# Optimization experiments

Hardware: AMD Instinct MI355X
Metric: run time of the kernel (lower is better)

The kernel has to match this reference:

```python
import jax, jax.numpy as jnp
import numpy as np

DECAY = 0.99
EPS = 1e-05


def setup_inputs() -> dict:
    key = jax.random.key(0)
    k1, k2 = jax.random.split(key)
    B, C, H, W = 16, 64, 32, 32
    K = 8192
    z_e = jax.random.normal(k1, (B, C, H, W), dtype=jnp.float32)
    embedding = jax.random.normal(k2, (K, C), dtype=jnp.float32)
    cluster_size = jnp.zeros((K,), dtype=jnp.float32)
    embedding_avg = embedding  # initialized as a clone of the codebook
    return {"z_e": z_e, "embedding": embedding, "cluster_size": cluster_size,
            "embedding_avg": embedding_avg}


def reference(z_e, embedding, cluster_size, embedding_avg):
    B, C, H, W = z_e.shape
    K = embedding.shape[0]
    # [N, C] tokens
    z_flat = jnp.transpose(z_e, (0, 2, 3, 1)).reshape(-1, C)
    d = ((z_flat * z_flat).sum(-1, keepdims=True)
         - 2.0 * (z_flat @ embedding.T)
         + (embedding * embedding).sum(-1))
    indices = jnp.argmin(d, axis=1)  # [N] int
    z_q_flat = embedding[indices]    # [N, C]
    z_q = jnp.transpose(z_q_flat.reshape(B, H, W, C), (0, 3, 1, 2))
    # EMA codebook update (training path); one-hot matmuls expressed as segment sums
    counts = jax.ops.segment_sum(jnp.ones(z_flat.shape[0], dtype=z_flat.dtype),
                                 indices, num_segments=K)            # encodings.sum(0)
    dw = jax.ops.segment_sum(z_flat, indices, num_segments=K)        # encodings.T @ z_flat
    new_cluster_size = DECAY * cluster_size + (1.0 - DECAY) * counts
    new_embedding_avg = DECAY * embedding_avg + (1.0 - DECAY) * dw
    n = new_cluster_size.sum()
    cs = (new_cluster_size + EPS) / (n + K * EPS) * n
    new_embedding = new_embedding_avg / cs[:, None]
    # straight-through estimator
    z_q_st = z_e + jax.lax.stop_gradient(z_q - z_e)
    return (z_q_st, indices.reshape(B, H * W), z_q,
            new_embedding, new_cluster_size, new_embedding_avg)
```

## Files before the change

### kernel.cpp

```cpp
#include <hip/hip_runtime.h>

#define DECAYF 0.99f
#define OMDF   0.01f
#define TAU    6.0e-3f

typedef unsigned int u32;
typedef unsigned long long u64;
typedef __attribute__((ext_vector_type(8))) short bf16x8;
typedef __attribute__((ext_vector_type(16))) float f32x16;

#define EN_OFF     0
#define EFRAG_OFF  32768
#define IDX_OFF    32768
#define LIST_OFF   98304
#define CELL_OFF   163840
#define BEST1_OFF  2129920
#define BEST2_OFF  4227072
#define CNT_OFF    5275648

__device__ __forceinline__ u64 enc_pair(float s, int idx) {
  u32 u = __float_as_uint(s);
  u = (u & 0x80000000u) ? ~u : (u | 0x80000000u);
  return ((u64)u << 32) | (u32)(~idx);
}
__device__ __forceinline__ float dec_score(u64 e) {
  u32 u = (u32)(e >> 32);
  u = (u & 0x80000000u) ? (u & 0x7fffffffu) : ~u;
  return __uint_as_float(u);
}
__device__ __forceinline__ int dec_idx(u64 e) { return (int)(~(u32)e); }
__device__ __forceinline__ unsigned short f2bf(float f) {
  u32 u = __float_as_uint(f);
  u += 0x7fffu + ((u >> 16) & 1u);
  return (unsigned short)(u >> 16);
}
__device__ __forceinline__ float exact_dot(const float* __restrict__ sx,
                                           const float* __restrict__ emb, int k) {
  const float4* e = (const float4*)(emb + (size_t)k * 64);
  float a = 0.f;
#pragma unroll
  for (int q = 0; q < 16; ++q) {
    float4 v = e[q];
    a = fmaf(sx[4 * q],     v.x, a);
    a = fmaf(sx[4 * q + 1], v.y, a);
    a = fmaf(sx[4 * q + 2], v.z, a);
    a = fmaf(sx[4 * q + 3], v.w, a);
  }
  return a;
}

__global__ __launch_bounds__(256) void k_en_eprep(const float* __restrict__ emb,
                                                  float* __restrict__ en,
                                                  unsigned char* __restrict__ efrag,
                                                  int* __restrict__ cnt,
                                                  float* __restrict__ nsum) {
  int tid = blockIdx.x * 256 + threadIdx.x;
  if (tid == 0) { *cnt = 0; *nsum = 0.f; }
  int k = tid >> 4, q = tid & 15;
  float4 v = ((const float4*)emb)[tid];
  int kstep = q >> 2, h = (q >> 1) & 1, j0 = (q & 1) * 4;
  int tile = k >> 5, n32 = k & 31;
  ushort4 hi, lo;
  hi.x = f2bf(v.x); lo.x = f2bf(v.x - __uint_as_float((u32)hi.x << 16));
  hi.y = f2bf(v.y); lo.y = f2bf(v.y - __uint_as_float((u32)hi.y << 16));
  hi.z = f2bf(v.z); lo.z = f2bf(v.z - __uint_as_float((u32)hi.z << 16));
  hi.w = f2bf(v.w); lo.w = f2bf(v.w - __uint_as_float((u32)hi.w << 16));
  size_t off = (size_t)tile * 8192 + (size_t)(kstep * 2) * 1024
             + (size_t)h * 512 + (size_t)n32 * 16 + (size_t)j0 * 2;
  *(ushort4*)(efrag + off)        = hi;
  *(ushort4*)(efrag + off + 1024) = lo;
  float s = v.x * v.x + v.y * v.y + v.z * v.z + v.w * v.w;
  s += __shfl_xor(s, 1, 16);
  s += __shfl_xor(s, 2, 16);
  s += __shfl_xor(s, 4, 16);
  s += __shfl_xor(s, 8, 16);
  if (q == 0) en[k] = 0.5f * s;
}

__global__ __launch_bounds__(256) void k_init(const float* __restrict__ cs_in,
                                              const float* __restrict__ avg_in,
                                              float* __restrict__ out4,
                                              float* __restrict__ out5,
                                              float* __restrict__ nsum) {
  int tid = blockIdx.x * 256 + threadIdx.x;
  if (tid < 131072) {
    float4 v = ((const float4*)avg_in)[tid];
    v.x *= DECAYF; v.y *= DECAYF; v.z *= DECAYF; v.w *= DECAYF;
    ((float4*)out5)[tid] = v;
  } else {
    int t = tid - 131072;
    float4 v = ((const float4*)cs_in)[t];
    v.x *= DECAYF; v.y *= DECAYF; v.z *= DECAYF; v.w *= DECAYF;
    ((float4*)out4)[t] = v;
    float s = v.x + v.y + v.z + v.w;
    s += __shfl_xor(s, 1, 64);
    s += __shfl_xor(s, 2, 64);
    s += __shfl_xor(s, 4, 64);
    s += __shfl_xor(s, 8, 64);
    s += __shfl_xor(s, 16, 64);
    s += __shfl_xor(s, 32, 64);
    if ((threadIdx.x & 63) == 0) atomicAdd(nsum, s);
  }
}

__global__ __launch_bounds__(256) void k_argmin_mfma(
    const float* __restrict__ z_e, const unsigned char* __restrict__ efrag,
    const float* __restrict__ en, u64* __restrict__ best1,
    float* __restrict__ best2) {
  alignas(16) __shared__ unsigned char sbuf[16384];
  const int tb = blockIdx.x >> 4;
  const int sl = blockIdx.x & 15;
  const int wave = threadIdx.x >> 6, lane = threadIdx.x & 63;
  const int h = lane >> 5, m = lane & 31;
  const int token0 = tb * 128 + wave * 32;

  bf16x8 ahi[4], alo[4];
  {
    const int token = token0 + m;
    const float* zp = z_e + ((size_t)(token >> 10) << 16) + (token & 1023);
#pragma unroll
    for (int ks = 0; ks < 4; ++ks) {
#pragma unroll
      for (int j = 0; j < 8; ++j) {
        int c = ks * 16 + h * 8 + j;
        float x = zp[(size_t)c << 10];
        unsigned short xh = f2bf(x);
        ahi[ks][j] = (short)xh;
        alo[ks][j] = (short)f2bf(x - __uint_as_float((u32)xh << 16));
      }
    }
  }
  float b1[16], b2[16];
#pragma unroll
  for (int r = 0; r < 16; ++r) { b1[r] = -3.0e38f; b2[r] = -3.0e38f; }

  const int scb = sl * 512;
  const unsigned char* gbase0 = efrag + (size_t)scb * 256;
  for (int ib = 0; ib < 8; ++ib) {
    const unsigned char* g = gbase0 + (size_t)ib * 16384 + (size_t)wave * 4096;
#pragma unroll
    for (int it = 0; it < 4; ++it) {
      __builtin_amdgcn_global_load_lds(
          (const __attribute__((address_space(1))) u32*)(g + it * 1024 + lane * 16),
          (__attribute__((address_space(3))) u32*)(sbuf + wave * 4096 + it * 1024),
          16, 0, 0);
    }
    __syncthreads();
#pragma unroll
    for (int t32 = 0; t32 < 2; ++t32) {
      const int t = ib * 2 + t32;
      const float negen = -en[scb + t * 32 + m];
      f32x16 acc;
#pragma unroll
      for (int r = 0; r < 16; ++r) acc[r] = negen;
      const unsigned char* sb = sbuf + t32 * 8192 + h * 512 + m * 16;
#pragma unroll
      for (int ks = 0; ks < 4; ++ks) {
        bf16x8 bh = *(const bf16x8*)(sb + (size_t)(ks * 2 + 0) * 1024);
        bf16x8 bl = *(const bf16x8*)(sb + (size_t)(ks * 2 + 1) * 1024);
        acc = __builtin_amdgcn_mfma_f32_32x32x16_bf16(ahi[ks], bh, acc, 0, 0, 0);
        acc = __builtin_amdgcn_mfma_f32_32x32x16_bf16(alo[ks], bh, acc, 0, 0, 0);
        acc = __builtin_amdgcn_mfma_f32_32x32x16_bf16(ahi[ks], bl, acc, 0, 0, 0);
      }
      const u32 emb6 = (u32)(63 - t);
#pragma unroll
      for (int r = 0; r < 16; ++r) {
        float f = __uint_as_float((__float_as_uint(acc[r]) & 0xFFFFFFC0u) | emb6);
        b2[r] = __builtin_amdgcn_fmed3f(f, b1[r], b2[r]);
        b1[r] = fmaxf(b1[r], f);
      }
    }
    __syncthreads();
  }
  int mi[16];
#pragma unroll
  for (int r = 0; r < 16; ++r) mi[r] = m;
#pragma unroll
  for (int st = 1; st < 32; st <<= 1) {
#pragma unroll
    for (int r = 0; r < 16; ++r) {
      float ob1 = __shfl_xor(b1[r], st, 64);
      float ob2 = __shfl_xor(b2[r], st, 64);
      int omi = __shfl_xor(mi[r], st, 64);
      bool ogt = ob1 > b1[r];
      b2[r] = fmaxf(fminf(b1[r], ob1), fmaxf(b2[r], ob2));
      mi[r] = ogt ? omi : mi[r];
      b1[r] = fmaxf(b1[r], ob1);
    }
  }
  if (m == 0) {
#pragma unroll
    for (int r = 0; r < 16; ++r) {
      int row = (r & 3) + 8 * (r >> 2) + 4 * h;
      int token = token0 + row;
      int t = 63 - (int)(__float_as_uint(b1[r]) & 63u);
      int gcode = scb + t * 32 + mi[r];
      best1[token * 16 + sl] = enc_pair(b1[r], gcode);
      best2[token * 16 + sl] = b2[r];
    }
  }
}

__global__ __launch_bounds__(256) void k_resolve(const u64* __restrict__ best1,
                                                 const float* __restrict__ best2,
                                                 int* __restrict__ idxa,
                                                 int* __restrict__ list,
                                                 int* __restrict__ cnt) {
  int n = blockIdx.x * 256 + threadIdx.x;
  const u64* bp = best1 + (size_t)n * 16;
  const float* sp = best2 + (size_t)n * 16;
  u64 e[16];
#pragma unroll
  for (int s = 0; s < 16; ++s) e[s] = bp[s];
  u64 top = e[0];
#pragma unroll
  for (int s = 1; s < 16; ++s) top = e[s] > top ? e[s] : top;
  float second = -3.0e38f;
#pragma unroll
  for (int s = 0; s < 16; ++s) second = fmaxf(second, sp[s]);
#pragma unroll
  for (int s = 0; s < 16; ++s)
    if (e[s] != top) second = fmaxf(second, dec_score(e[s]));
  idxa[n] = dec_idx(top);
  if (dec_score(top) - second < TAU) {
    int p = atomicAdd(cnt, 1);
    list[p] = n;
  }
}

__global__ __launch_bounds__(256) void k_fixup(const float* __restrict__ z_e,
                                               const float* __restrict__ emb,
                                               const float* __restrict__ en,
                                               const u64* __restrict__ best1,
                                               const float* __restrict__ best2,
                                               const int* __restrict__ list,
                                               const int* __restrict__ cnt,
                                               u64* __restrict__ cell) {
  __shared__ float sx[64];
  __shared__ u64 esh[16];
  __shared__ float b2sh[16];
  __shared__ int cand[16];
  __shared__ int fsl[16];
  __shared__ int ncand, nfsl;
  __shared__ u64 red;
  int count = *cnt;
  for (int i = blockIdx.x; i < count; i += gridDim.x) {
    int n = list[i];
    __syncthreads();
    if (threadIdx.x == 0) { ncand = 0; nfsl = 0; red = 0ull; }
    if (threadIdx.x < 16) {
      esh[threadIdx.x]  = best1[(size_t)n * 16 + threadIdx.x];
      b2sh[threadIdx.x] = best2[(size_t)n * 16 + threadIdx.x];
    }
    if (threadIdx.x < 64) {
      sx[threadIdx.x] = z_e[((size_t)(n >> 10) << 16)
                            + ((size_t)threadIdx.x << 10) + (n & 1023)];
    }
    __syncthreads();
    u64 top = esh[0];
#pragma unroll
    for (int s = 1; s < 16; ++s) top = esh[s] > top ? esh[s] : top;
    float theta = dec_score(top) - TAU;
    if (threadIdx.x < 16) {
      int s = threadIdx.x;
      if (dec_score(esh[s]) >= theta) {
        int p = atomicAdd(&ncand, 1);
        cand[p] = dec_idx(esh[s]);
      }
      if (b2sh[s] >= theta) {
        int p = atomicAdd(&nfsl, 1);
        fsl[p] = s;
      }
    }
    __syncthreads();
    u64 myb = 0ull;
    if (threadIdx.x < ncand) {
      int k = cand[threadIdx.x];
      float a = exact_dot(sx, emb, k) - en[k];
      myb = enc_pair(a, k);
    }
    int nf = nfsl;
    for (int f = 0; f < nf; ++f) {
      int s = fsl[f];
      int k0 = s * 512 + threadIdx.x;
      int k1 = k0 + 256;
      float a0 = exact_dot(sx, emb, k0) - en[k0];
      float a1 = exact_dot(sx, emb, k1) - en[k1];
      u64 m0 = enc_pair(a0, k0), m1 = enc_pair(a1, k1);
      u64 mm = m0 > m1 ? m0 : m1;
      myb = mm > myb ? mm : myb;
    }
    if (myb) atomicMax(&red, myb);
    __syncthreads();
    if (threadIdx.x == 0) cell[i] = red;
  }
}

__global__ __launch_bounds__(256) void k_post(const int* __restrict__ list,
                                              const int* __restrict__ cnt,
                                              const u64* __restrict__ cell,
                                              int* __restrict__ idxa) {
  int i = blockIdx.x * 256 + threadIdx.x;
  if (i < *cnt) idxa[list[i]] = dec_idx(cell[i]);
}

__global__ __launch_bounds__(256) void k_scatter(const float* __restrict__ z_e,
                                                 const int* __restrict__ idxa,
                                                 float* __restrict__ out4,
                                                 float* __restrict__ out5) {
  int tid = blockIdx.x * 256 + threadIdx.x;
  int n = tid >> 6, c = tid & 63;
  int idx = idxa[n];
  int b = n >> 10, hw = n & 1023;
  float x = z_e[((size_t)b << 16) + ((size_t)c << 10) + hw];
  atomicAdd(out5 + (size_t)idx * 64 + c, OMDF * x);
  if (c == 0) atomicAdd(out4 + idx, OMDF);
}

__global__ __launch_bounds__(256) void k_gather(const float* __restrict__ z_e,
                                                const float* __restrict__ emb,
                                                const int* __restrict__ idxa,
                                                float* __restrict__ out0,
                                                float* __restrict__ out1,
                                                float* __restrict__ out2) {
  int tid = blockIdx.x * 256 + threadIdx.x;
  int hw4 = tid & 255;
  int c   = (tid >> 8) & 63;
  int b   = tid >> 14;
  int n0  = (b << 10) + (hw4 << 2);
  size_t off = ((size_t)b << 16) + ((size_t)c << 10) + ((size_t)hw4 << 2);
  float4 z = *(const float4*)(z_e + off);
  int i0 = idxa[n0], i1 = idxa[n0 + 1], i2 = idxa[n0 + 2], i3 = idxa[n0 + 3];
  float4 q;
  q.x = emb[(size_t)i0 * 64 + c];
  q.y = emb[(size_t)i1 * 64 + c];
  q.z = emb[(size_t)i2 * 64 + c];
  q.w = emb[(size_t)i3 * 64 + c];
  float4 st;
  st.x = z.x + (q.x - z.x);
  st.y = z.y + (q.y - z.y);
  st.z = z.z + (q.z - z.z);
  st.w = z.w + (q.w - z.w);
  *(float4*)(out2 + off) = q;
  *(float4*)(out0 + off) = st;
  if (c == 0) {
    float4 f = make_float4((float)i0, (float)i1, (float)i2, (float)i3);
    *(float4*)(out1 + n0) = f;
  }
}

__global__ __launch_bounds__(256) void k_final(const float* __restrict__ out4,
                                               const float* __restrict__ out5,
                                               const float* __restrict__ nsum,
                                               float* __restrict__ out3) {
  int tid = blockIdx.x * 256 + threadIdx.x;
  int k = tid >> 4;
  double nn  = (double)*nsum + 163.84;
  double ncs = (double)out4[k];
  double cs  = (ncs + 1e-5) / (nn + 8192.0 * 1e-5) * nn;
  float inv  = (float)(1.0 / cs);
  float4 v = ((const float4*)out5)[tid];
  v.x *= inv; v.y *= inv; v.z *= inv; v.w *= inv;
  ((float4*)out3)[tid] = v;
}

extern "C" void kernel_launch(void* const* d_in, const int* in_sizes, int n_in,
                              void* d_out, int out_size, void* d_ws, size_t ws_size,
                              hipStream_t stream) {
  const float* z_e    = (const float*)d_in[0];
  const float* emb    = (const float*)d_in[1];
  const float* cs_in  = (const float*)d_in[2];
  const float* avg_in = (const float*)d_in[3];

  float* out  = (float*)d_out;
  float* out0 = out;
  float* out1 = out0 + 1048576;
  float* out2 = out1 + 16384;
  float* out3 = out2 + 1048576;
  float* out4 = out3 + 524288;
  float* out5 = out4 + 8192;

  char* ws = (char*)d_ws;
  float* en            = (float*)(ws + EN_OFF);
  unsigned char* efrag = (unsigned char*)(ws + EFRAG_OFF);
  u64* best1           = (u64*)(ws + BEST1_OFF);
  float* best2         = (float*)(ws + BEST2_OFF);
  int* idxa            = (int*)(ws + IDX_OFF);
  int* list            = (int*)(ws + LIST_OFF);
  int* cnt             = (int*)(ws + CNT_OFF);
  float* nsum          = (float*)(ws + CNT_OFF + 4);
  u64* cell            = (u64*)(ws + CELL_OFF);

  k_en_eprep   <<<512,  256, 0, stream>>>(emb, en, efrag, cnt, nsum);
  k_init       <<<520,  256, 0, stream>>>(cs_in, avg_in, out4, out5, nsum);
  k_argmin_mfma<<<2048, 256, 0, stream>>>(z_e, efrag, en, best1, best2);
  k_resolve    <<<64,   256, 0, stream>>>(best1, best2, idxa, list, cnt);
  k_fixup      <<<1024, 256, 0, stream>>>(z_e, emb, en, best1, best2, list, cnt, cell);
  k_post       <<<64,   256, 0, stream>>>(list, cnt, cell, idxa);
  k_scatter    <<<4096, 256, 0, stream>>>(z_e, idxa, out4, out5);
  k_gather     <<<1024, 256, 0, stream>>>(z_e, emb, idxa, out0, out1, out2);
  k_final      <<<512,  256, 0, stream>>>(out4, out5, nsum, out3);
}
```

Baseline: 173.0 us.

## Fuse prep kernels, pre-split z into bf16 fragments, double-buffer codebook tiles

Merges the codebook prep and EMA init kernels into one launch, which also pre-converts z_e into hi/lo bf16 MFMA fragments stored in the out0 buffer. The argmin kernel now covers 1024 codes per block instead of 512, halving the slice count from 16 to 8. It double-buffers the LDS codebook tiles so the next tile's loads overlap the current MFMAs, and caches the code norms in LDS. The best1/best2 layout becomes slice-major for coalesced writes. The aim is to cut strided z_e loads, launch overhead and load/compute stalls, at the cost of an extra pass writing zfrag and a larger per-block fixup scan.

```diff
diff --git a/kernel.cpp b/kernel.cpp
--- a/kernel.cpp
+++ b/kernel.cpp
@@ -15,8 +15,8 @@
 #define LIST_OFF   98304
 #define CELL_OFF   163840
 #define BEST1_OFF  2129920
-#define BEST2_OFF  4227072
-#define CNT_OFF    5275648
+#define BEST2_OFF  3178496
+#define CNT_OFF    3702784
 
 __device__ __forceinline__ u64 enc_pair(float s, int idx) {
   u32 u = __float_as_uint(s);
@@ -49,111 +49,143 @@
   return a;
 }
 
-__global__ __launch_bounds__(256) void k_en_eprep(const float* __restrict__ emb,
-                                                  float* __restrict__ en,
-                                                  unsigned char* __restrict__ efrag,
-                                                  int* __restrict__ cnt,
-                                                  float* __restrict__ nsum) {
-  int tid = blockIdx.x * 256 + threadIdx.x;
-  if (tid == 0) { *cnt = 0; *nsum = 0.f; }
-  int k = tid >> 4, q = tid & 15;
-  float4 v = ((const float4*)emb)[tid];
-  int kstep = q >> 2, h = (q >> 1) & 1, j0 = (q & 1) * 4;
-  int tile = k >> 5, n32 = k & 31;
-  ushort4 hi, lo;
-  hi.x = f2bf(v.x); lo.x = f2bf(v.x - __uint_as_float((u32)hi.x << 16));
-  hi.y = f2bf(v.y); lo.y = f2bf(v.y - __uint_as_float((u32)hi.y << 16));
-  hi.z = f2bf(v.z); lo.z = f2bf(v.z - __uint_as_float((u32)hi.z << 16));
-  hi.w = f2bf(v.w); lo.w = f2bf(v.w - __uint_as_float((u32)hi.w << 16));
-  size_t off = (size_t)tile * 8192 + (size_t)(kstep * 2) * 1024
-             + (size_t)h * 512 + (size_t)n32 * 16 + (size_t)j0 * 2;
-  *(ushort4*)(efrag + off)        = hi;
-  *(ushort4*)(efrag + off + 1024) = lo;
-  float s = v.x * v.x + v.y * v.y + v.z * v.z + v.w * v.w;
-  s += __shfl_xor(s, 1, 16);
-  s += __shfl_xor(s, 2, 16);
-  s += __shfl_xor(s, 4, 16);
-  s += __shfl_xor(s, 8, 16);
-  if (q == 0) en[k] = 0.5f * s;
-}
-
-__global__ __launch_bounds__(256) void k_init(const float* __restrict__ cs_in,
+__global__ __launch_bounds__(256) void k_prep(const float* __restrict__ emb,
+                                              const float* __restrict__ cs_in,
                                               const float* __restrict__ avg_in,
+                                              const float* __restrict__ z_e,
+                                              float* __restrict__ en,
+                                              unsigned char* __restrict__ efrag,
+                                              unsigned char* __restrict__ zfrag,
                                               float* __restrict__ out4,
                                               float* __restrict__ out5,
+                                              int* __restrict__ cnt,
                                               float* __restrict__ nsum) {
-  int tid = blockIdx.x * 256 + threadIdx.x;
-  if (tid < 131072) {
-    float4 v = ((const float4*)avg_in)[tid];
-    v.x *= DECAYF; v.y *= DECAYF; v.z *= DECAYF; v.w *= DECAYF;
-    ((float4*)out5)[tid] = v;
-  } else {
-    int t = tid - 131072;
-    float4 v = ((const float4*)cs_in)[t];
-    v.x *= DECAYF; v.y *= DECAYF; v.z *= DECAYF; v.w *= DECAYF;
-    ((float4*)out4)[t] = v;
-    float s = v.x + v.y + v.z + v.w;
+  __shared__ float warr[4];
+  int bid = blockIdx.x;
+  if (bid < 512) {
+    int tid = bid * 256 + threadIdx.x;
+    if (tid == 0) *cnt = 0;
+    int k = tid >> 4, q = tid & 15;
+    float4 v = ((const float4*)emb)[tid];
+    int kstep = q >> 2, h = (q >> 1) & 1, j0 = (q & 1) * 4;
+    int tile = k >> 5, n32 = k & 31;
+    ushort4 hi, lo;
+    hi.x = f2bf(v.x); lo.x = f2bf(v.x - __uint_as_float((u32)hi.x << 16));
+    hi.y = f2bf(v.y); lo.y = f2bf(v.y - __uint_as_float((u32)hi.y << 16));
+    hi.z = f2bf(v.z); lo.z = f2bf(v.z - __uint_as_float((u32)hi.z << 16));
+    hi.w = f2bf(v.w); lo.w = f2bf(v.w - __uint_as_float((u32)hi.w << 16));
+    size_t off = (size_t)tile * 8192 + (size_t)(kstep * 2) * 1024
+               + (size_t)h * 512 + (size_t)n32 * 16 + (size_t)j0 * 2;
+    *(ushort4*)(efrag + off)        = hi;
+    *(ushort4*)(efrag + off + 1024) = lo;
+    float s = v.x * v.x + v.y * v.y + v.z * v.z + v.w * v.w;
+    s += __shfl_xor(s, 1, 16);
+    s += __shfl_xor(s, 2, 16);
+    s += __shfl_xor(s, 4, 16);
+    s += __shfl_xor(s, 8, 16);
+    if (q == 0) en[k] = 0.5f * s;
+  } else if (bid < 1031) {
+    int tid = (bid - 512) * 256 + threadIdx.x;
+    if (tid < 131072) {
+      float4 v = ((const float4*)avg_in)[tid];
+      v.x *= DECAYF; v.y *= DECAYF; v.z *= DECAYF; v.w *= DECAYF;
+      ((float4*)out5)[tid] = v;
+    }
+  } else if (bid == 1031) {
+    int thr = threadIdx.x;
+    float s = 0.f;
+#pragma unroll
+    for (int q = 0; q < 8; ++q) {
+      int idx = q * 256 + thr;
+      float4 v = ((const float4*)cs_in)[idx];
+      v.x *= DECAYF; v.y *= DECAYF; v.z *= DECAYF; v.w *= DECAYF;
+      ((float4*)out4)[idx] = v;
+      s += v.x + v.y + v.z + v.w;
+    }
     s += __shfl_xor(s, 1, 64);
     s += __shfl_xor(s, 2, 64);
     s += __shfl_xor(s, 4, 64);
     s += __shfl_xor(s, 8, 64);
     s += __shfl_xor(s, 16, 64);
     s += __shfl_xor(s, 32, 64);
-    if ((threadIdx.x & 63) == 0) atomicAdd(nsum, s);
+    if ((thr & 63) == 0) warr[thr >> 6] = s;
+    __syncthreads();
+    if (thr == 0) *nsum = warr[0] + warr[1] + warr[2] + warr[3];
+  } else {
+    int t = (bid - 1032) * 256 + threadIdx.x;
+    int q4 = t & 255, c = (t >> 8) & 63, b = t >> 14;
+    size_t off = ((size_t)b << 16) + ((size_t)c << 10) + ((size_t)q4 << 2);
+    float4 v = *(const float4*)(z_e + off);
+    int tg = b * 32 + (q4 >> 3);
+    int mb = (q4 & 7) * 4;
+    int ks = c >> 4, hh = (c >> 3) & 1, j = c & 7;
+    size_t base = (size_t)tg * 8192 + (size_t)ks * 1024 + (size_t)hh * 512
+                + (size_t)mb * 16 + (size_t)j * 2;
+    float xs[4] = {v.x, v.y, v.z, v.w};
+#pragma unroll
+    for (int i = 0; i < 4; ++i) {
+      unsigned short hi = f2bf(xs[i]);
+      unsigned short lo = f2bf(xs[i] - __uint_as_float((u32)hi << 16));
+      *(unsigned short*)(zfrag + base + (size_t)i * 16)        = hi;
+      *(unsigned short*)(zfrag + base + (size_t)i * 16 + 4096) = lo;
+    }
   }
 }
 
 __global__ __launch_bounds__(256) void k_argmin_mfma(
-    const float* __restrict__ z_e, const unsigned char* __restrict__ efrag,
+    const unsigned char* __restrict__ zfrag,
+    const unsigned char* __restrict__ efrag,
     const float* __restrict__ en, u64* __restrict__ best1,
     float* __restrict__ best2) {
-  alignas(16) __shared__ unsigned char sbuf[16384];
-  const int tb = blockIdx.x >> 4;
-  const int sl = blockIdx.x & 15;
+  alignas(16) __shared__ unsigned char sbuf[2][16384];
+  __shared__ float sen[1024];
+  const int tb = blockIdx.x >> 3;
+  const int sl = blockIdx.x & 7;
   const int wave = threadIdx.x >> 6, lane = threadIdx.x & 63;
   const int h = lane >> 5, m = lane & 31;
   const int token0 = tb * 128 + wave * 32;
+  const int scb = sl << 10;
+
+  ((float4*)sen)[threadIdx.x] = ((const float4*)(en + scb))[threadIdx.x];
 
   bf16x8 ahi[4], alo[4];
   {
-    const int token = token0 + m;
-    const float* zp = z_e + ((size_t)(token >> 10) << 16) + (token & 1023);
+    const unsigned char* zb = zfrag + ((size_t)(tb * 4 + wave)) * 8192
+                            + (size_t)h * 512 + (size_t)m * 16;
 #pragma unroll
     for (int ks = 0; ks < 4; ++ks) {
-#pragma unroll
-      for (int j = 0; j < 8; ++j) {
-        int c = ks * 16 + h * 8 + j;
-        float x = zp[(size_t)c << 10];
-        unsigned short xh = f2bf(x);
-        ahi[ks][j] = (short)xh;
-        alo[ks][j] = (short)f2bf(x - __uint_as_float((u32)xh << 16));
-      }
+      ahi[ks] = *(const bf16x8*)(zb + (size_t)ks * 1024);
+      alo[ks] = *(const bf16x8*)(zb + (size_t)ks * 1024 + 4096);
     }
   }
   float b1[16], b2[16];
 #pragma unroll
   for (int r = 0; r < 16; ++r) { b1[r] = -3.0e38f; b2[r] = -3.0e38f; }
 
-  const int scb = sl * 512;
   const unsigned char* gbase0 = efrag + (size_t)scb * 256;
-  for (int ib = 0; ib < 8; ++ib) {
+  auto stage = [&](int ib, int buf) {
     const unsigned char* g = gbase0 + (size_t)ib * 16384 + (size_t)wave * 4096;
 #pragma unroll
     for (int it = 0; it < 4; ++it) {
       __builtin_amdgcn_global_load_lds(
           (const __attribute__((address_space(1))) u32*)(g + it * 1024 + lane * 16),
-          (__attribute__((address_space(3))) u32*)(sbuf + wave * 4096 + it * 1024),
+          (__attribute__((address_space(3))) u32*)(&sbuf[buf][wave * 4096 + it * 1024]),
           16, 0, 0);
     }
-    __syncthreads();
+  };
+  stage(0, 0);
+  for (int ib = 0; ib < 16; ++ib) {
+    __syncthreads();
+    if (ib < 15) stage(ib + 1, (ib + 1) & 1);
+    const unsigned char* sb0 = &sbuf[ib & 1][0];
 #pragma unroll
     for (int t32 = 0; t32 < 2; ++t32) {
       const int t = ib * 2 + t32;
-      const float negen = -en[scb + t * 32 + m];
+      const float negen = -sen[t * 32 + m];
       f32x16 acc;
 #pragma unroll
       for (int r = 0; r < 16; ++r) acc[r] = negen;
-      const unsigned char* sb = sbuf + t32 * 8192 + h * 512 + m * 16;
+      const unsigned char* sb = sb0 + t32 * 8192 + h * 512 + m * 16;
 #pragma unroll
       for (int ks = 0; ks < 4; ++ks) {
         bf16x8 bh = *(const bf16x8*)(sb + (size_t)(ks * 2 + 0) * 1024);
@@ -170,7 +202,6 @@
         b1[r] = fmaxf(b1[r], f);
       }
     }
-    __syncthreads();
   }
   int mi[16];
 #pragma unroll
@@ -195,8 +226,8 @@
       int token = token0 + row;
       int t = 63 - (int)(__float_as_uint(b1[r]) & 63u);
       int gcode = scb + t * 32 + mi[r];
-      best1[token * 16 + sl] = enc_pair(b1[r], gcode);
-      best2[token * 16 + sl] = b2[r];
+      best1[(size_t)sl * 16384 + token] = enc_pair(b1[r], gcode);
+      best2[(size_t)sl * 16384 + token] = b2[r];
     }
   }
 }
@@ -207,19 +238,21 @@
                                                  int* __restrict__ list,
                                                  int* __restrict__ cnt) {
   int n = blockIdx.x * 256 + threadIdx.x;
-  const u64* bp = best1 + (size_t)n * 16;
-  const float* sp = best2 + (size_t)n * 16;
-  u64 e[16];
-#pragma unroll
-  for (int s = 0; s < 16; ++s) e[s] = bp[s];
+  u64 e[8];
+  float sp[8];
+#pragma unroll
+  for (int s = 0; s < 8; ++s) {
+    e[s]  = best1[(size_t)s * 16384 + n];
+    sp[s] = best2[(size_t)s * 16384 + n];
+  }
   u64 top = e[0];
 #pragma unroll
-  for (int s = 1; s < 16; ++s) top = e[s] > top ? e[s] : top;
+  for (int s = 1; s < 8; ++s) top = e[s] > top ? e[s] : top;
   float second = -3.0e38f;
 #pragma unroll
-  for (int s = 0; s < 16; ++s) second = fmaxf(second, sp[s]);
-#pragma unroll
-  for (int s = 0; s < 16; ++s)
+  for (int s = 0; s < 8; ++s) second = fmaxf(second, sp[s]);
+#pragma unroll
+  for (int s = 0; s < 8; ++s)
     if (e[s] != top) second = fmaxf(second, dec_score(e[s]));
   idxa[n] = dec_idx(top);
   if (dec_score(top) - second < TAU) {
@@ -237,10 +270,10 @@
                                                const int* __restrict__ cnt,
                                                u64* __restrict__ cell) {
   __shared__ float sx[64];
-  __shared__ u64 esh[16];
-  __shared__ float b2sh[16];
-  __shared__ int cand[16];
-  __shared__ int fsl[16];
+  __shared__ u64 esh[8];
+  __shared__ float b2sh[8];
+  __shared__ int cand[8];
+  __shared__ int fsl[8];
   __shared__ int ncand, nfsl;
   __shared__ u64 red;
   int count = *cnt;
@@ -248,9 +281,9 @@
     int n = list[i];
     __syncthreads();
     if (threadIdx.x == 0) { ncand = 0; nfsl = 0; red = 0ull; }
-    if (threadIdx.x < 16) {
-      esh[threadIdx.x]  = best1[(size_t)n * 16 + threadIdx.x];
-      b2sh[threadIdx.x] = best2[(size_t)n * 16 + threadIdx.x];
+    if (threadIdx.x < 8) {
+      esh[threadIdx.x]  = best1[(size_t)threadIdx.x * 16384 + n];
+      b2sh[threadIdx.x] = best2[(size_t)threadIdx.x * 16384 + n];
     }
     if (threadIdx.x < 64) {
       sx[threadIdx.x] = z_e[((size_t)(n >> 10) << 16)
@@ -259,9 +292,9 @@
     __syncthreads();
     u64 top = esh[0];
 #pragma unroll
-    for (int s = 1; s < 16; ++s) top = esh[s] > top ? esh[s] : top;
+    for (int s = 1; s < 8; ++s) top = esh[s] > top ? esh[s] : top;
     float theta = dec_score(top) - TAU;
-    if (threadIdx.x < 16) {
+    if (threadIdx.x < 8) {
       int s = threadIdx.x;
       if (dec_score(esh[s]) >= theta) {
         int p = atomicAdd(&ncand, 1);
@@ -282,12 +315,15 @@
     int nf = nfsl;
     for (int f = 0; f < nf; ++f) {
       int s = fsl[f];
-      int k0 = s * 512 + threadIdx.x;
-      int k1 = k0 + 256;
-      float a0 = exact_dot(sx, emb, k0) - en[k0];
-      float a1 = exact_dot(sx, emb, k1) - en[k1];
-      u64 m0 = enc_pair(a0, k0), m1 = enc_pair(a1, k1);
-      u64 mm = m0 > m1 ? m0 : m1;
+      int k0 = (s << 10) + threadIdx.x;
+      float a0 = exact_dot(sx, emb, k0)       - en[k0];
+      float a1 = exact_dot(sx, emb, k0 + 256) - en[k0 + 256];
+      float a2 = exact_dot(sx, emb, k0 + 512) - en[k0 + 512];
+      float a3 = exact_dot(sx, emb, k0 + 768) - en[k0 + 768];
+      u64 m0 = enc_pair(a0, k0),       m1 = enc_pair(a1, k0 + 256);
+      u64 m2 = enc_pair(a2, k0 + 512), m3 = enc_pair(a3, k0 + 768);
+      u64 ma = m0 > m1 ? m0 : m1, mb = m2 > m3 ? m2 : m3;
+      u64 mm = ma > mb ? ma : mb;
       myb = mm > myb ? mm : myb;
     }
     if (myb) atomicMax(&red, myb);
@@ -390,10 +426,11 @@
   int* cnt             = (int*)(ws + CNT_OFF);
   float* nsum          = (float*)(ws + CNT_OFF + 4);
   u64* cell            = (u64*)(ws + CELL_OFF);
-
-  k_en_eprep   <<<512,  256, 0, stream>>>(emb, en, efrag, cnt, nsum);
-  k_init       <<<520,  256, 0, stream>>>(cs_in, avg_in, out4, out5, nsum);
-  k_argmin_mfma<<<2048, 256, 0, stream>>>(z_e, efrag, en, best1, best2);
+  unsigned char* zfrag = (unsigned char*)out0;
+
+  k_prep       <<<2056, 256, 0, stream>>>(emb, cs_in, avg_in, z_e, en, efrag,
+                                          zfrag, out4, out5, cnt, nsum);
+  k_argmin_mfma<<<1024, 256, 0, stream>>>(zfrag, efrag, en, best1, best2);
   k_resolve    <<<64,   256, 0, stream>>>(best1, best2, idxa, list, cnt);
   k_fixup      <<<1024, 256, 0, stream>>>(z_e, emb, en, best1, best2, list, cnt, cell);
   k_post       <<<64,   256, 0, stream>>>(list, cnt, cell, idxa);
```

Measured after the change: 182.3 us. 5.4% more time.
